# Kernel optimization log

Hardware: AMD Instinct MI355X
Metric: run time of the kernel (lower is better)

Reference implementation:

```python
import jax, jax.numpy as jnp
import numpy as np

B, N, D = 32, 65536, 16
M, H, OUT = 32, 64, 3  # m_model_output, hidden width, i_model output


def setup_inputs() -> dict:
    key = jax.random.key(0)
    ks = jax.random.split(key, 5)
    s = lambda fan_in: 1.0 / np.sqrt(fan_in)
    return {
        "inputs": jax.random.normal(ks[0], (B, N, D), dtype=jnp.float32),
        "mw1": jax.random.normal(ks[1], (D, H), dtype=jnp.float32) * s(D),
        "mb1": jnp.zeros((H,), dtype=jnp.float32),
        "mw2": jax.random.normal(ks[2], (H, M), dtype=jnp.float32) * s(H),
        "mb2": jnp.zeros((M,), dtype=jnp.float32),
        "iw1": jax.random.normal(ks[3], (M + 1, H), dtype=jnp.float32) * s(M + 1),
        "ib1": jnp.zeros((H,), dtype=jnp.float32),
        "iw2": jax.random.normal(ks[4], (H, OUT), dtype=jnp.float32) * s(H),
        "ib2": jnp.zeros((OUT,), dtype=jnp.float32),
    }


def reference(inputs, mw1, mb1, mw2, mb2, iw1, ib1, iw2, ib2):
    # m_model: per-node MLP producing messages [B, N, M]
    h = jax.nn.relu(jnp.einsum("bnd,dh->bnh", inputs, mw1) + mb1)
    messages = jnp.einsum("bnh,hm->bnm", h, mw2) + mb2
    # concat(messages[:j], messages[j:]) is identity -> sum over ALL nodes
    msg_sum = jnp.sum(messages, axis=1, keepdims=True)  # [B, 1, M]
    msg_sum = jnp.broadcast_to(msg_sum, (inputs.shape[0], inputs.shape[1], messages.shape[-1]))
    # append each node's last scalar feature -> [B, N, M+1]
    feat = jnp.concatenate([msg_sum, inputs[..., -1:]], axis=-1)
    # i_model: per-node MLP -> [B, N, OUT]
    g = jax.nn.relu(jnp.einsum("bnf,fh->bnh", feat, iw1) + ib1)
    out = jnp.einsum("bnh,ho->bno", g, iw2) + ib2
    return out
```

## Files before the change

kernel.cpp:

```cpp
#include <hip/hip_runtime.h>
#include <hip/hip_bf16.h>

#define Bb   32
#define Nn   65536
#define Dd   16
#define Hh   64
#define Mm   32
#define OUTn 3

#define NPW   256
#define WPB_N (Nn / NPW)
#define TPB   256
#define NSEG  65

typedef __attribute__((ext_vector_type(8)))  __bf16 bf16x8;
typedef __attribute__((ext_vector_type(4)))  __bf16 bf16x4;
typedef __attribute__((ext_vector_type(16))) float  f32x16;
typedef __attribute__((ext_vector_type(4)))  float  f32x4;

static __device__ inline void split_bf(float w, __bf16& hi, __bf16& lo) {
    hi = (__bf16)w;
    lo = (__bf16)(w - (float)hi);
}

__global__ __launch_bounds__(TPB) void k_mphase(
    const float* __restrict__ in, const float* __restrict__ mw1,
    const float* __restrict__ mb1, float* __restrict__ partials,
    __bf16* __restrict__ xlast)
{
    const int lane = threadIdx.x & 63;
    const int l31  = lane & 31;
    const int half = lane >> 5;
    const int wid  = blockIdx.x * (TPB / 64) + (threadIdx.x >> 6);
    const size_t node0 = (size_t)wid * NPW;

    bf16x8 bhiA, bloA, bhiB, bloB;
#pragma unroll
    for (int e = 0; e < 8; ++e) {
        const int k = 8 * half + e;
        __bf16 h, l;
        split_bf(mw1[k * Hh + l31], h, l);        bhiA[e] = h; bloA[e] = l;
        split_bf(mw1[k * Hh + 32 + l31], h, l);   bhiB[e] = h; bloB[e] = l;
    }
    const float biasA = mb1[l31];
    const float biasB = mb1[32 + l31];

    float hsumA = 0.f, hsumB = 0.f;
    const float* __restrict__ inw = in + node0 * Dd + (size_t)l31 * Dd + 8 * half;

    f32x4 c0 = *(const f32x4*)(inw);
    f32x4 c1 = *(const f32x4*)(inw + 4);

#pragma unroll 1
    for (int s = 0; s < NPW / 32; ++s) {
        f32x4 n0, n1;
        if (s < NPW / 32 - 1) {
            const float* apn = inw + (size_t)(s + 1) * 32 * Dd;
            n0 = *(const f32x4*)(apn);
            n1 = *(const f32x4*)(apn + 4);
        }

        bf16x8 a;
        a[0] = (__bf16)c0[0]; a[1] = (__bf16)c0[1];
        a[2] = (__bf16)c0[2]; a[3] = (__bf16)c0[3];
        a[4] = (__bf16)c1[0]; a[5] = (__bf16)c1[1];
        a[6] = (__bf16)c1[2]; a[7] = (__bf16)c1[3];

        f32x16 z{};
        f32x16 accA = __builtin_amdgcn_mfma_f32_32x32x16_bf16(a, bloA, z, 0, 0, 0);
        accA        = __builtin_amdgcn_mfma_f32_32x32x16_bf16(a, bhiA, accA, 0, 0, 0);
        f32x16 accB = __builtin_amdgcn_mfma_f32_32x32x16_bf16(a, bloB, z, 0, 0, 0);
        accB        = __builtin_amdgcn_mfma_f32_32x32x16_bf16(a, bhiB, accB, 0, 0, 0);

#pragma unroll
        for (int r = 0; r < 16; ++r) {
            accA[r] = fmaxf(accA[r] + biasA, 0.f);
            accB[r] = fmaxf(accB[r] + biasB, 0.f);
        }
#pragma unroll
        for (int st = 8; st >= 1; st >>= 1)
#pragma unroll
            for (int r = 0; r < st; ++r) {
                accA[r] += accA[r + st];
                accB[r] += accB[r + st];
            }
        hsumA += accA[0]; hsumB += accB[0];

        float x15 = __shfl_xor(c1[3], 32, 64);
        if (lane < 32) xlast[node0 + (size_t)s * 32 + lane] = (__bf16)x15;

        c0 = n0; c1 = n1;
    }

    hsumA += __shfl_xor(hsumA, 32, 64);
    hsumB += __shfl_xor(hsumB, 32, 64);
    partials[(size_t)wid * Hh + lane] = (lane < 32) ? hsumA : hsumB;
}

__global__ __launch_bounds__(256) void k_combine(
    const float* __restrict__ partials,
    const float* __restrict__ mw2, const float* __restrict__ mb2,
    const float* __restrict__ iw1, const float* __restrict__ ib1,
    const float* __restrict__ iw2, const float* __restrict__ ib2,
    float* __restrict__ knotsG, float* __restrict__ segG)
{
    __shared__ float red[4][Hh];
    __shared__ float sHs[Hh], sMs[Mm], sBase[Hh], sW[Hh], sKn[Hh], sSort[Hh];
    __shared__ float sIw2[Hh * OUTn];
    const int b = blockIdx.x;
    const int t = threadIdx.x;
    const int h = t & 63, slice = t >> 6;

    float s = 0.f;
    const float* p = partials + ((size_t)b * WPB_N + slice * 64) * Hh + h;
#pragma unroll 8
    for (int w = 0; w < 64; ++w) s += p[(size_t)w * Hh];
    red[slice][h] = s;
    for (int i = t; i < Hh * OUTn; i += 256) sIw2[i] = iw2[i];
    __syncthreads();

    if (t < Hh) sHs[t] = red[0][t] + red[1][t] + red[2][t] + red[3][t];
    __syncthreads();

    if (t < Mm) {
        float v = (float)Nn * mb2[t];
        for (int hh = 0; hh < Hh; ++hh) v = fmaf(sHs[hh], mw2[hh * Mm + t], v);
        sMs[t] = v;
    }
    __syncthreads();

    if (t < Hh) {
        float bs = ib1[t];
        for (int m = 0; m < Mm; ++m) bs = fmaf(sMs[m], iw1[m * Hh + t], bs);
        float w = iw1[Mm * Hh + t];
        sBase[t] = bs; sW[t] = w;
        float k = (w != 0.f) ? (-bs / w) : 1e15f;
        if (!(fabsf(k) < 1e15f)) k = 1e15f;
        sKn[t] = k;
    }
    __syncthreads();

    if (t < Hh) {
        float k = sKn[t];
        int r = 0;
        for (int j = 0; j < Hh; ++j) {
            float kj = sKn[j];
            r += (kj < k || (kj == k && j < t)) ? 1 : 0;
        }
        sSort[r] = k;
    }
    __syncthreads();

    if (t < Hh) knotsG[(size_t)b * Hh + t] = sSort[t];
    if (t < NSEG) {
        float lo = (t == 0)  ? sSort[0] - 1.0f      : sSort[t - 1];
        float hi = (t == Hh) ? sSort[Hh - 1] + 1.0f : sSort[t];
        float m  = 0.5f * lo + 0.5f * hi;
        float A0 = ib2[0], A1 = ib2[1], A2 = ib2[2], B0 = 0.f, B1 = 0.f, B2 = 0.f;
        for (int hh = 0; hh < Hh; ++hh) {
            float bs = sBase[hh], w = sW[hh];
            if (fmaf(w, m, bs) > 0.f) {
                A0 = fmaf(bs, sIw2[hh * 3 + 0], A0);
                A1 = fmaf(bs, sIw2[hh * 3 + 1], A1);
                A2 = fmaf(bs, sIw2[hh * 3 + 2], A2);
                B0 = fmaf(w,  sIw2[hh * 3 + 0], B0);
                B1 = fmaf(w,  sIw2[hh * 3 + 1], B1);
                B2 = fmaf(w,  sIw2[hh * 3 + 2], B2);
            }
        }
        float* sg = segG + (size_t)b * 6 * NSEG;
        sg[0 * NSEG + t] = A0; sg[1 * NSEG + t] = A1; sg[2 * NSEG + t] = A2;
        sg[3 * NSEG + t] = B0; sg[4 * NSEG + t] = B1; sg[5 * NSEG + t] = B2;
    }
}

__global__ __launch_bounds__(TPB) void k_iphase(
    const __bf16* __restrict__ xl, const float* __restrict__ knotsG,
    const float* __restrict__ segG, float* __restrict__ out)
{
    __shared__ __align__(16) float sK[Hh];
    __shared__ float sT[6 * NSEG];
    const int t = threadIdx.x;
    const int b = blockIdx.x >> 6;

    if (t < Hh) sK[t] = knotsG[(size_t)b * Hh + t];
    for (int i = t; i < 6 * NSEG; i += TPB) sT[i] = segG[(size_t)b * 6 * NSEG + i];
    __syncthreads();

    const size_t n0 = ((size_t)blockIdx.x * TPB + t) * 4;
    bf16x4 xv = *(const bf16x4*)(xl + n0);
    float o[12];
#pragma unroll
    for (int i = 0; i < 4; ++i) {
        const float x = (float)xv[i];
        int pos = 0;
#pragma unroll
        for (int st = 32; st >= 1; st >>= 1)
            pos += (sK[pos + st - 1] < x) ? st : 0;
        pos += (sK[pos] < x) ? 1 : 0;
        o[3 * i + 0] = fmaf(sT[3 * NSEG + pos], x, sT[0 * NSEG + pos]);
        o[3 * i + 1] = fmaf(sT[4 * NSEG + pos], x, sT[1 * NSEG + pos]);
        o[3 * i + 2] = fmaf(sT[5 * NSEG + pos], x, sT[2 * NSEG + pos]);
    }
    f32x4* po = (f32x4*)(out + n0 * 3);
    po[0] = f32x4{o[0], o[1], o[2],  o[3]};
    po[1] = f32x4{o[4], o[5], o[6],  o[7]};
    po[2] = f32x4{o[8], o[9], o[10], o[11]};
}

extern "C" void kernel_launch(void* const* d_in, const int* in_sizes, int n_in,
                              void* d_out, int out_size, void* d_ws, size_t ws_size,
                              hipStream_t stream) {
    const float* in  = (const float*)d_in[0];
    const float* mw1 = (const float*)d_in[1];
    const float* mb1 = (const float*)d_in[2];
    const float* mw2 = (const float*)d_in[3];
    const float* mb2 = (const float*)d_in[4];
    const float* iw1 = (const float*)d_in[5];
    const float* ib1 = (const float*)d_in[6];
    const float* iw2 = (const float*)d_in[7];
    const float* ib2 = (const float*)d_in[8];
    float* out = (float*)d_out;

    char* ws = (char*)d_ws;
    const size_t PART_SZ = (size_t)Bb * WPB_N * Hh * sizeof(float);
    float*  partials = (float*)(ws);
    float*  knotsG   = (float*)(ws + PART_SZ);
    float*  segG     = (float*)(ws + PART_SZ + 8192);
    __bf16* xl       = (__bf16*)(ws + PART_SZ + 131072);

    const int nblocks = (Bb * Nn / NPW) / (TPB / 64);
    hipLaunchKernelGGL(k_mphase, dim3(nblocks), dim3(TPB), 0, stream,
                       in, mw1, mb1, partials, xl);
    hipLaunchKernelGGL(k_combine, dim3(Bb), dim3(256), 0, stream,
                       partials, mw2, mb2, iw1, ib1, iw2, ib2, knotsG, segG);
    hipLaunchKernelGGL(k_iphase, dim3((Bb * Nn) / (TPB * 4)), dim3(TPB), 0, stream,
                       xl, knotsG, segG, out);
}
```

Before: 53.50 us.

## Stage m-phase input through LDS with async global_load_lds double buffering

The m-phase kernel now has each block copy 256-node chunks of the input into a double-buffered LDS tile using global_load_lds, with the next chunk's copy issued before the current one is computed. Each block covers 2048 nodes, so there are half as many blocks and each wave handles 512 nodes instead of 256. k_combine is changed to sum the resulting 32 partials per slice. The aim is fully coalesced, asynchronous loads and more memory-level parallelism; the cost is block-wide barriers each chunk, LDS use that limits occupancy, and fewer blocks in flight.

After: 52.28 us. -2.3%, faster.

```diff
diff --git a/kernel.cpp b/kernel.cpp
--- a/kernel.cpp
+++ b/kernel.cpp
@@ -8,10 +8,13 @@
 #define Mm   32
 #define OUTn 3
 
-#define NPW   256
-#define WPB_N (Nn / NPW)
-#define TPB   256
-#define NSEG  65
+#define TPB    256
+#define CHUNK  256
+#define NCH    8
+#define SEGN   (CHUNK * NCH)
+#define NWAVES ((Bb * Nn) / 512)
+#define WPB    (NWAVES / Bb)
+#define NSEG   65
 
 typedef __attribute__((ext_vector_type(8)))  __bf16 bf16x8;
 typedef __attribute__((ext_vector_type(4)))  __bf16 bf16x4;
@@ -21,6 +24,12 @@
 static __device__ inline void split_bf(float w, __bf16& hi, __bf16& lo) {
     hi = (__bf16)w;
     lo = (__bf16)(w - (float)hi);
+}
+
+typedef const __attribute__((address_space(1))) unsigned int gu32;
+typedef __attribute__((address_space(3))) unsigned int lu32;
+static __device__ __forceinline__ void gld16(const float* g, float* l) {
+    __builtin_amdgcn_global_load_lds((gu32*)g, (lu32*)l, 16, 0, 0);
 }
 
 __global__ __launch_bounds__(TPB) void k_mphase(
@@ -28,11 +37,14 @@
     const float* __restrict__ mb1, float* __restrict__ partials,
     __bf16* __restrict__ xlast)
 {
-    const int lane = threadIdx.x & 63;
+    __shared__ float lds[2][CHUNK * Dd];
+
+    const int tid  = threadIdx.x;
+    const int lane = tid & 63;
+    const int w    = tid >> 6;
     const int l31  = lane & 31;
     const int half = lane >> 5;
-    const int wid  = blockIdx.x * (TPB / 64) + (threadIdx.x >> 6);
-    const size_t node0 = (size_t)wid * NPW;
+    const size_t blk0 = (size_t)blockIdx.x * SEGN;
 
     bf16x8 bhiA, bloA, bhiB, bloB;
 #pragma unroll
@@ -46,54 +58,67 @@
     const float biasB = mb1[32 + l31];
 
     float hsumA = 0.f, hsumB = 0.f;
-    const float* __restrict__ inw = in + node0 * Dd + (size_t)l31 * Dd + 8 * half;
-
-    f32x4 c0 = *(const f32x4*)(inw);
-    f32x4 c1 = *(const f32x4*)(inw + 4);
+
+    auto stage = [&](int bf, int c) {
+        const float* src = in + (blk0 + (size_t)c * CHUNK + tid) * Dd;
+#pragma unroll
+        for (int q = 0; q < 4; ++q)
+            gld16(src + q * 4, &lds[bf][(size_t)(q * CHUNK) * 4 + (size_t)w * 256]);
+    };
+
+    int cur = 0;
+    stage(0, 0);
+    __syncthreads();
 
 #pragma unroll 1
-    for (int s = 0; s < NPW / 32; ++s) {
-        f32x4 n0, n1;
-        if (s < NPW / 32 - 1) {
-            const float* apn = inw + (size_t)(s + 1) * 32 * Dd;
-            n0 = *(const f32x4*)(apn);
-            n1 = *(const f32x4*)(apn + 4);
+    for (int c = 0; c < NCH; ++c) {
+        if (c + 1 < NCH) stage(cur ^ 1, c + 1);
+
+#pragma unroll
+        for (int T = 0; T < 2; ++T) {
+            const int nb = w * 64 + T * 32 + l31;
+            const int q0 = half * 2;
+            f32x4 v0 = *(const f32x4*)&lds[cur][(size_t)(q0 * CHUNK + nb) * 4];
+            f32x4 v1 = *(const f32x4*)&lds[cur][(size_t)((q0 + 1) * CHUNK + nb) * 4];
+
+            bf16x8 a;
+            a[0] = (__bf16)v0[0]; a[1] = (__bf16)v0[1];
+            a[2] = (__bf16)v0[2]; a[3] = (__bf16)v0[3];
+            a[4] = (__bf16)v1[0]; a[5] = (__bf16)v1[1];
+            a[6] = (__bf16)v1[2]; a[7] = (__bf16)v1[3];
+
+            f32x16 z{};
+            f32x16 accA = __builtin_amdgcn_mfma_f32_32x32x16_bf16(a, bloA, z, 0, 0, 0);
+            accA        = __builtin_amdgcn_mfma_f32_32x32x16_bf16(a, bhiA, accA, 0, 0, 0);
+            f32x16 accB = __builtin_amdgcn_mfma_f32_32x32x16_bf16(a, bloB, z, 0, 0, 0);
+            accB        = __builtin_amdgcn_mfma_f32_32x32x16_bf16(a, bhiB, accB, 0, 0, 0);
+
+#pragma unroll
+            for (int r = 0; r < 16; ++r) {
+                accA[r] = fmaxf(accA[r] + biasA, 0.f);
+                accB[r] = fmaxf(accB[r] + biasB, 0.f);
+            }
+#pragma unroll
+            for (int st = 8; st >= 1; st >>= 1)
+#pragma unroll
+                for (int r = 0; r < st; ++r) {
+                    accA[r] += accA[r + st];
+                    accB[r] += accB[r + st];
+                }
+            hsumA += accA[0]; hsumB += accB[0];
+
+            float x15 = __shfl_xor(v1[3], 32, 64);
+            if (lane < 32)
+                xlast[blk0 + (size_t)c * CHUNK + w * 64 + T * 32 + lane] = (__bf16)x15;
         }
 
-        bf16x8 a;
-        a[0] = (__bf16)c0[0]; a[1] = (__bf16)c0[1];
-        a[2] = (__bf16)c0[2]; a[3] = (__bf16)c0[3];
-        a[4] = (__bf16)c1[0]; a[5] = (__bf16)c1[1];
-        a[6] = (__bf16)c1[2]; a[7] = (__bf16)c1[3];
-
-        f32x16 z{};
-        f32x16 accA = __builtin_amdgcn_mfma_f32_32x32x16_bf16(a, bloA, z, 0, 0, 0);
-        accA        = __builtin_amdgcn_mfma_f32_32x32x16_bf16(a, bhiA, accA, 0, 0, 0);
-        f32x16 accB = __builtin_amdgcn_mfma_f32_32x32x16_bf16(a, bloB, z, 0, 0, 0);
-        accB        = __builtin_amdgcn_mfma_f32_32x32x16_bf16(a, bhiB, accB, 0, 0, 0);
-
-#pragma unroll
-        for (int r = 0; r < 16; ++r) {
-            accA[r] = fmaxf(accA[r] + biasA, 0.f);
-            accB[r] = fmaxf(accB[r] + biasB, 0.f);
-        }
-#pragma unroll
-        for (int st = 8; st >= 1; st >>= 1)
-#pragma unroll
-            for (int r = 0; r < st; ++r) {
-                accA[r] += accA[r + st];
-                accB[r] += accB[r + st];
-            }
-        hsumA += accA[0]; hsumB += accB[0];
-
-        float x15 = __shfl_xor(c1[3], 32, 64);
-        if (lane < 32) xlast[node0 + (size_t)s * 32 + lane] = (__bf16)x15;
-
-        c0 = n0; c1 = n1;
+        __syncthreads();
+        cur ^= 1;
     }
 
     hsumA += __shfl_xor(hsumA, 32, 64);
     hsumB += __shfl_xor(hsumB, 32, 64);
+    const int wid = blockIdx.x * 4 + w;
     partials[(size_t)wid * Hh + lane] = (lane < 32) ? hsumA : hsumB;
 }
 
@@ -112,9 +137,9 @@
     const int h = t & 63, slice = t >> 6;
 
     float s = 0.f;
-    const float* p = partials + ((size_t)b * WPB_N + slice * 64) * Hh + h;
+    const float* p = partials + ((size_t)b * WPB + slice * 32) * Hh + h;
 #pragma unroll 8
-    for (int w = 0; w < 64; ++w) s += p[(size_t)w * Hh];
+    for (int ww = 0; ww < 32; ++ww) s += p[(size_t)ww * Hh];
     red[slice][h] = s;
     for (int i = t; i < Hh * OUTn; i += 256) sIw2[i] = iw2[i];
     __syncthreads();
@@ -223,13 +248,13 @@
     float* out = (float*)d_out;
 
     char* ws = (char*)d_ws;
-    const size_t PART_SZ = (size_t)Bb * WPB_N * Hh * sizeof(float);
+    const size_t PART_SZ = (size_t)NWAVES * Hh * sizeof(float);
     float*  partials = (float*)(ws);
     float*  knotsG   = (float*)(ws + PART_SZ);
     float*  segG     = (float*)(ws + PART_SZ + 8192);
     __bf16* xl       = (__bf16*)(ws + PART_SZ + 131072);
 
-    const int nblocks = (Bb * Nn / NPW) / (TPB / 64);
+    const int nblocks = (Bb * Nn) / SEGN;
     hipLaunchKernelGGL(k_mphase, dim3(nblocks), dim3(TPB), 0, stream,
                        in, mw1, mb1, partials, xl);
     hipLaunchKernelGGL(k_combine, dim3(Bb), dim3(256), 0, stream,
```

## Deepen load pipeline to four tiles in flight and double nodes per wave

Applied to the files above, without the earlier changes.

Each wave in the m-phase kernel now handles 512 nodes instead of 256. The loop keeps four tiles of input loads in flight through a rotating register set rather than prefetching a single next tile. This is meant to hide global-memory latency on a bandwidth-bound 134 MB read, and it halves the number of partial sums the combine kernel has to reduce. The cost is fewer waves, which lowers parallelism per CU, plus extra register pressure from the eight f32x4 buffers.

Measured after the change: 61.04 us. 1.14x slower.

```diff
diff --git a/kernel.cpp b/kernel.cpp
--- a/kernel.cpp
+++ b/kernel.cpp
@@ -8,7 +8,8 @@
 #define Mm   32
 #define OUTn 3
 
-#define NPW   256
+#define NPW   512
+#define NT    (NPW / 32)
 #define WPB_N (Nn / NPW)
 #define TPB   256
 #define NSEG  65
@@ -48,23 +49,17 @@
     float hsumA = 0.f, hsumB = 0.f;
     const float* __restrict__ inw = in + node0 * Dd + (size_t)l31 * Dd + 8 * half;
 
-    f32x4 c0 = *(const f32x4*)(inw);
-    f32x4 c1 = *(const f32x4*)(inw + 4);
-
-#pragma unroll 1
-    for (int s = 0; s < NPW / 32; ++s) {
-        f32x4 n0, n1;
-        if (s < NPW / 32 - 1) {
-            const float* apn = inw + (size_t)(s + 1) * 32 * Dd;
-            n0 = *(const f32x4*)(apn);
-            n1 = *(const f32x4*)(apn + 4);
-        }
-
+    f32x4 r0a, r0b, r1a, r1b, r2a, r2b, r3a, r3b;
+#define ISSUE(s, t)                                                  \
+    r##s##a = *(const f32x4*)(inw + (size_t)(t) * 512);              \
+    r##s##b = *(const f32x4*)(inw + (size_t)(t) * 512 + 4)
+
+    auto consume = [&](f32x4 va, f32x4 vb, int tile) {
         bf16x8 a;
-        a[0] = (__bf16)c0[0]; a[1] = (__bf16)c0[1];
-        a[2] = (__bf16)c0[2]; a[3] = (__bf16)c0[3];
-        a[4] = (__bf16)c1[0]; a[5] = (__bf16)c1[1];
-        a[6] = (__bf16)c1[2]; a[7] = (__bf16)c1[3];
+        a[0] = (__bf16)va[0]; a[1] = (__bf16)va[1];
+        a[2] = (__bf16)va[2]; a[3] = (__bf16)va[3];
+        a[4] = (__bf16)vb[0]; a[5] = (__bf16)vb[1];
+        a[6] = (__bf16)vb[2]; a[7] = (__bf16)vb[3];
 
         f32x16 z{};
         f32x16 accA = __builtin_amdgcn_mfma_f32_32x32x16_bf16(a, bloA, z, 0, 0, 0);
@@ -86,11 +81,22 @@
             }
         hsumA += accA[0]; hsumB += accB[0];
 
-        float x15 = __shfl_xor(c1[3], 32, 64);
-        if (lane < 32) xlast[node0 + (size_t)s * 32 + lane] = (__bf16)x15;
-
-        c0 = n0; c1 = n1;
-    }
+        float x15 = __shfl_xor(vb[3], 32, 64);
+        if (lane < 32)
+            xlast[node0 + (size_t)tile * 32 + lane] = (__bf16)x15;
+    };
+
+    ISSUE(0, 0); ISSUE(1, 1); ISSUE(2, 2); ISSUE(3, 3);
+
+#pragma unroll 1
+    for (int g = 0; g < NT / 4; ++g) {
+        const int t0 = g * 4;
+        consume(r0a, r0b, t0 + 0); if (g < NT / 4 - 1) { ISSUE(0, t0 + 4); }
+        consume(r1a, r1b, t0 + 1); if (g < NT / 4 - 1) { ISSUE(1, t0 + 5); }
+        consume(r2a, r2b, t0 + 2); if (g < NT / 4 - 1) { ISSUE(2, t0 + 6); }
+        consume(r3a, r3b, t0 + 3); if (g < NT / 4 - 1) { ISSUE(3, t0 + 7); }
+    }
+#undef ISSUE
 
     hsumA += __shfl_xor(hsumA, 32, 64);
     hsumB += __shfl_xor(hsumB, 32, 64);
@@ -112,9 +118,9 @@
     const int h = t & 63, slice = t >> 6;
 
     float s = 0.f;
-    const float* p = partials + ((size_t)b * WPB_N + slice * 64) * Hh + h;
+    const float* p = partials + ((size_t)b * WPB_N + slice * 32) * Hh + h;
 #pragma unroll 8
-    for (int w = 0; w < 64; ++w) s += p[(size_t)w * Hh];
+    for (int ww = 0; ww < 32; ++ww) s += p[(size_t)ww * Hh];
     red[slice][h] = s;
     for (int i = t; i < Hh * OUTn; i += 256) sIw2[i] = iw2[i];
     __syncthreads();
@@ -229,7 +235,9 @@
     float*  segG     = (float*)(ws + PART_SZ + 8192);
     __bf16* xl       = (__bf16*)(ws + PART_SZ + 131072);
 
-    const int nblocks = (Bb * Nn / NPW) / (TPB / 64);
+    const int nwaves  = (Bb * Nn) / NPW;
+    const int nblocks = nwaves / (TPB / 64);
+
     hipLaunchKernelGGL(k_mphase, dim3(nblocks), dim3(TPB), 0, stream,
                        in, mw1, mb1, partials, xl);
     hipLaunchKernelGGL(k_combine, dim3(Bb), dim3(256), 0, stream,
```
